# Kernel tuning notes

Measured on AMD Instinct MI355X. Metric: run time of the kernel, lower is better.

Reference implementation:

```python
import jax, jax.numpy as jnp
import numpy as np

B, HW, C, H = 4, 2048, 768, 8
HD = C // H  # 96


def _rotate_half_interleaved(t):
    # t: [..., HD]; pairs (t1, t2) at even/odd positions -> (-t2, t1) interleaved
    t1 = t[..., ::2]
    t2 = t[..., 1::2]
    return jnp.stack([-t2, t1], axis=-1).reshape(t.shape)


def setup_inputs() -> dict:
    key = jax.random.key(0)
    kx, kq, kp, kb = jax.random.split(key, 4)
    x = jax.random.normal(kx, (B, HW, C), dtype=jnp.float32)
    # standard interleaved RoPE tables: freq repeated pairwise along head_dim
    inv_freq = 1.0 / (10000.0 ** (np.arange(0, HD, 2, dtype=np.float32) / HD))  # [HD/2]
    angles = np.arange(HW, dtype=np.float32)[:, None] * inv_freq[None, :]        # [HW, HD/2]
    angles = np.repeat(angles, 2, axis=-1)                                        # [HW, HD]
    cos = jnp.asarray(np.cos(angles), dtype=jnp.float32)
    sin = jnp.asarray(np.sin(angles), dtype=jnp.float32)
    Wqkv = jax.random.normal(kq, (3 * C, C), dtype=jnp.float32) * (C ** -0.5)
    Wproj = jax.random.normal(kp, (C, C), dtype=jnp.float32) * (C ** -0.5)
    bproj = jnp.zeros((C,), dtype=jnp.float32)
    return {"x": x, "cos": cos, "sin": sin, "Wqkv": Wqkv, "Wproj": Wproj, "bproj": bproj}


def reference(x, cos, sin, Wqkv, Wproj, bproj):
    Bv, hw, Cv = x.shape
    scale = HD ** -0.5
    qkv = x @ Wqkv.T                                  # [B, hw, 3C]
    qkv = qkv.reshape(Bv, hw, 3, H, HD).transpose(2, 0, 3, 1, 4)  # [3, B, H, hw, HD]
    q, k, v = qkv[0], qkv[1], qkv[2]
    # RoPE: broadcast cos/sin [hw, HD] over [B, H, hw, HD]
    cosb = cos[None, None, :, :]
    sinb = sin[None, None, :, :]
    q = q * cosb + _rotate_half_interleaved(q) * sinb
    k = k * cosb + _rotate_half_interleaved(k) * sinb
    attn = jnp.einsum('bhqd,bhkd->bhqk', q, k) * scale
    attn = jax.nn.softmax(attn, axis=-1)
    out = jnp.einsum('bhqk,bhkd->bhqd', attn, v)      # [B, H, hw, HD]
    out = out.transpose(0, 2, 1, 3).reshape(Bv, hw, Cv)
    return out @ Wproj.T + bproj
```

## Files before the change

### kernel.cpp

```cpp
#include <hip/hip_runtime.h>
#include <hip/hip_bf16.h>
#include <math.h>

#define Bc  4
#define HWc 2048
#define Cc  768
#define Hc  8
#define HDc 96

typedef short bf16x8 __attribute__((ext_vector_type(8)));
typedef float f32x4  __attribute__((ext_vector_type(4)));

static __device__ __forceinline__ unsigned short f2bf(float x) {
    __hip_bfloat16 h = __float2bfloat16(x);
    return *reinterpret_cast<unsigned short*>(&h);
}

#define GLOBAL_AS(p) ((const __attribute__((address_space(1))) void*)(p))
#define LDS_AS(p)    ((__attribute__((address_space(3))) void*)(p))

__global__ __launch_bounds__(256) void cast_bf16(
    const float* __restrict__ src, unsigned short* __restrict__ dst, int n4)
{
    int i = blockIdx.x * 256 + threadIdx.x;
    if (i < n4) {
        float4 v = ((const float4*)src)[i];
        ushort4 p;
        p.x = f2bf(v.x); p.y = f2bf(v.y); p.z = f2bf(v.z); p.w = f2bf(v.w);
        ((ushort4*)dst)[i] = p;
    }
}

__global__ __launch_bounds__(256) void qkv_mfma_T(
    const unsigned short* __restrict__ Wb, const unsigned short* __restrict__ xb,
    const float* __restrict__ cs, const float* __restrict__ sn,
    unsigned short* __restrict__ qo, unsigned short* __restrict__ ko,
    unsigned short* __restrict__ vt)
{
    __shared__ unsigned short Al[128 * 32];
    __shared__ unsigned short Bl[128 * 32];
    const int tid  = threadIdx.x;
    const int lane = tid & 63;
    const int w    = tid >> 6;
    const int c    = lane & 15, qd = lane >> 4;
    const int wm   = w & 1, wn = w >> 1;
    const int m0   = blockIdx.y << 7;
    const int n0   = blockIdx.x << 7;

    const int srow = (w << 5) + (lane >> 2);
    const int sseg = (lane & 3) << 3;
    const unsigned short* Ag = Wb + (size_t)(m0 + srow) * Cc + sseg;
    const unsigned short* Bg = xb + (size_t)(n0 + srow) * Cc + sseg;
    unsigned short* Adst = &Al[(w << 5) * 32];
    unsigned short* Bdst = &Bl[(w << 5) * 32];

    f32x4 acc[4][4];
    #pragma unroll
    for (int i = 0; i < 4; i++)
        #pragma unroll
        for (int j = 0; j < 4; j++) acc[i][j] = (f32x4)0.f;

    for (int k0 = 0; k0 < Cc; k0 += 32) {
        __syncthreads();
        __builtin_amdgcn_global_load_lds(GLOBAL_AS(Ag + k0),            LDS_AS(Adst),            16, 0, 0);
        __builtin_amdgcn_global_load_lds(GLOBAL_AS(Ag + 16 * Cc + k0),  LDS_AS(Adst + 16 * 32),  16, 0, 0);
        __builtin_amdgcn_global_load_lds(GLOBAL_AS(Bg + k0),            LDS_AS(Bdst),            16, 0, 0);
        __builtin_amdgcn_global_load_lds(GLOBAL_AS(Bg + 16 * Cc + k0),  LDS_AS(Bdst + 16 * 32),  16, 0, 0);
        __syncthreads();

        bf16x8 af[4], bfr[4];
        #pragma unroll
        for (int mt = 0; mt < 4; mt++)
            af[mt] = *(const bf16x8*)&Al[((wm << 6) + mt * 16 + c) * 32 + qd * 8];
        #pragma unroll
        for (int nt = 0; nt < 4; nt++)
            bfr[nt] = *(const bf16x8*)&Bl[((wn << 6) + nt * 16 + c) * 32 + qd * 8];
        #pragma unroll
        for (int mt = 0; mt < 4; mt++)
            #pragma unroll
            for (int nt = 0; nt < 4; nt++)
                acc[mt][nt] = __builtin_amdgcn_mfma_f32_16x16x32_bf16(
                    af[mt], bfr[nt], acc[mt][nt], 0, 0, 0);
    }

    const int which = m0 / Cc;
    const int m0l = m0 - which * Cc;
    const float qs = 0.10206207261596577f;

    if (which == 2) {
        #pragma unroll
        for (int mt = 0; mt < 4; mt++) {
            const int c0 = m0l + (wm << 6) + mt * 16 + (qd << 2);
            const int h = c0 / HDc, d = c0 % HDc;
            #pragma unroll
            for (int nt = 0; nt < 4; nt++) {
                const int t = n0 + (wn << 6) + nt * 16 + c;
                const int b = t >> 11, tt = t & (HWc - 1);
                const size_t base = ((size_t)((b * Hc + h) * HDc + d)) * HWc + tt;
                #pragma unroll
                for (int r = 0; r < 4; r++)
                    vt[base + (size_t)r * HWc] = f2bf(acc[mt][nt][r]);
            }
        }
    } else {
        unsigned short* dst = which ? ko : qo;
        const float sc = which ? 1.0f : qs;
        #pragma unroll
        for (int mt = 0; mt < 4; mt++) {
            const int c0 = m0l + (wm << 6) + mt * 16 + (qd << 2);
            const int h = c0 / HDc, d = c0 % HDc;
            #pragma unroll
            for (int nt = 0; nt < 4; nt++) {
                const int t = n0 + (wn << 6) + nt * 16 + c;
                const int b = t >> 11, tt = t & (HWc - 1);
                const float4 c4 = *(const float4*)&cs[tt * HDc + d];
                const float4 s4 = *(const float4*)&sn[tt * HDc + d];
                float o0 = (acc[mt][nt][0] * c4.x - acc[mt][nt][1] * s4.x) * sc;
                float o1 = (acc[mt][nt][1] * c4.y + acc[mt][nt][0] * s4.y) * sc;
                float o2 = (acc[mt][nt][2] * c4.z - acc[mt][nt][3] * s4.z) * sc;
                float o3 = (acc[mt][nt][3] * c4.w + acc[mt][nt][2] * s4.w) * sc;
                ushort4 pk;
                pk.x = f2bf(o0); pk.y = f2bf(o1); pk.z = f2bf(o2); pk.w = f2bf(o3);
                *(ushort4*)&dst[((size_t)(b * Hc + h) * HWc + tt) * HDc + d] = pk;
            }
        }
    }
}

__global__ __launch_bounds__(256) void attn_flash(
    const unsigned short* __restrict__ qg, const unsigned short* __restrict__ kg,
    const unsigned short* __restrict__ vtg, unsigned short* __restrict__ ob)
{
    __shared__ unsigned short Ks[64][104];
    __shared__ unsigned short Vt[96][104];
    __shared__ unsigned short Pt[4][32][104];

    const int tid  = threadIdx.x;
    const int lane = tid & 63;
    const int w    = tid >> 6;
    const int c    = lane & 15;
    const int qd   = lane >> 4;
    const int bh   = blockIdx.x;
    const int b    = bh >> 3, h = bh & 7;
    const int q0   = blockIdx.y << 7;

    const unsigned short* kb  = kg  + (size_t)bh * HWc * HDc;
    const unsigned short* vtb = vtg + (size_t)bh * HDc * HWc;

    bf16x8 qt[2][3];
    #pragma unroll
    for (int nt = 0; nt < 2; nt++) {
        const unsigned short* qr =
            qg + ((size_t)bh * HWc + q0 + w * 32 + nt * 16 + c) * HDc + qd * 8;
        #pragma unroll
        for (int ks = 0; ks < 3; ks++)
            qt[nt][ks] = *(const bf16x8*)(qr + ks * 32);
    }

    f32x4 oacc[6][2];
    #pragma unroll
    for (int mt = 0; mt < 6; mt++)
        #pragma unroll
        for (int nt = 0; nt < 2; nt++) oacc[mt][nt] = (f32x4)0.f;
    float lsum[2] = {0.f, 0.f};

    const int krow0 = tid / 12,       kseg0 = tid - krow0 * 12;
    const int krow1 = (tid + 256) / 12, kseg1 = (tid + 256) - krow1 * 12;
    const int krow2 = (tid + 512) / 12, kseg2 = (tid + 512) - krow2 * 12;
    uint4 kreg[3], vreg[3];

    {
        const unsigned short* kc = kb;
        kreg[0] = *(const uint4*)(kc + krow0 * HDc + kseg0 * 8);
        kreg[1] = *(const uint4*)(kc + krow1 * HDc + kseg1 * 8);
        kreg[2] = *(const uint4*)(kc + krow2 * HDc + kseg2 * 8);
        const unsigned short* vc = vtb;
        #pragma unroll
        for (int it = 0; it < 3; it++) {
            int idx = tid + (it << 8);
            int row = idx >> 3, seg = idx & 7;
            vreg[it] = *(const uint4*)(vc + (size_t)row * HWc + seg * 8);
        }
    }

    for (int ck = 0; ck < 32; ck++) {
        __syncthreads();
        *(uint4*)&Ks[krow0][kseg0 * 8] = kreg[0];
        *(uint4*)&Ks[krow1][kseg1 * 8] = kreg[1];
        *(uint4*)&Ks[krow2][kseg2 * 8] = kreg[2];
        #pragma unroll
        for (int it = 0; it < 3; it++) {
            int idx = tid + (it << 8);
            int row = idx >> 3, seg = idx & 7;
            *(uint4*)&Vt[row][seg * 8] = vreg[it];
        }
        __syncthreads();

        if (ck + 1 < 32) {
            const unsigned short* kc = kb + (size_t)((ck + 1) << 6) * HDc;
            kreg[0] = *(const uint4*)(kc + krow0 * HDc + kseg0 * 8);
            kreg[1] = *(const uint4*)(kc + krow1 * HDc + kseg1 * 8);
            kreg[2] = *(const uint4*)(kc + krow2 * HDc + kseg2 * 8);
            const unsigned short* vc = vtb + ((ck + 1) << 6);
            #pragma unroll
            for (int it = 0; it < 3; it++) {
                int idx = tid + (it << 8);
                int row = idx >> 3, seg = idx & 7;
                vreg[it] = *(const uint4*)(vc + (size_t)row * HWc + seg * 8);
            }
        }

        f32x4 sacc[4][2];
        #pragma unroll
        for (int mt = 0; mt < 4; mt++)
            #pragma unroll
            for (int nt = 0; nt < 2; nt++) sacc[mt][nt] = (f32x4)0.f;
        #pragma unroll
        for (int mt = 0; mt < 4; mt++)
            #pragma unroll
            for (int ks = 0; ks < 3; ks++) {
                bf16x8 af = *(const bf16x8*)&Ks[mt * 16 + c][ks * 32 + qd * 8];
                sacc[mt][0] = __builtin_amdgcn_mfma_f32_16x16x32_bf16(
                    af, qt[0][ks], sacc[mt][0], 0, 0, 0);
                sacc[mt][1] = __builtin_amdgcn_mfma_f32_16x16x32_bf16(
                    af, qt[1][ks], sacc[mt][1], 0, 0, 0);
            }

        #pragma unroll
        for (int nt = 0; nt < 2; nt++) {
            float rs = 0.f;
            #pragma unroll
            for (int mt = 0; mt < 4; mt++)
                #pragma unroll
                for (int r = 0; r < 4; r++) {
                    float p = __expf(sacc[mt][nt][r]);
                    sacc[mt][nt][r] = p;
                    rs += p;
                }
            rs += __shfl_xor(rs, 16);
            rs += __shfl_xor(rs, 32);
            lsum[nt] += rs;
        }

        #pragma unroll
        for (int nt = 0; nt < 2; nt++)
            #pragma unroll
            for (int mt = 0; mt < 4; mt++) {
                __hip_bfloat162 p01 = __float22bfloat162_rn(
                    float2{sacc[mt][nt][0], sacc[mt][nt][1]});
                __hip_bfloat162 p23 = __float22bfloat162_rn(
                    float2{sacc[mt][nt][2], sacc[mt][nt][3]});
                uint2 pk;
                pk.x = *reinterpret_cast<unsigned int*>(&p01);
                pk.y = *reinterpret_cast<unsigned int*>(&p23);
                *(uint2*)&Pt[w][nt * 16 + c][mt * 16 + qd * 4] = pk;
            }
        bf16x8 pf[2][2];
        #pragma unroll
        for (int nt = 0; nt < 2; nt++)
            #pragma unroll
            for (int ks = 0; ks < 2; ks++)
                pf[nt][ks] = *(const bf16x8*)&Pt[w][nt * 16 + c][ks * 32 + qd * 8];

        #pragma unroll
        for (int mt = 0; mt < 6; mt++)
            #pragma unroll
            for (int ks = 0; ks < 2; ks++) {
                bf16x8 vf = *(const bf16x8*)&Vt[mt * 16 + c][ks * 32 + qd * 8];
                oacc[mt][0] = __builtin_amdgcn_mfma_f32_16x16x32_bf16(
                    vf, pf[0][ks], oacc[mt][0], 0, 0, 0);
                oacc[mt][1] = __builtin_amdgcn_mfma_f32_16x16x32_bf16(
                    vf, pf[1][ks], oacc[mt][1], 0, 0, 0);
            }
    }

    #pragma unroll
    for (int nt = 0; nt < 2; nt++) {
        const float linv = 1.0f / lsum[nt];
        unsigned short* orow =
            ob + ((size_t)(b * HWc + q0 + w * 32 + nt * 16 + c)) * Cc + h * HDc;
        #pragma unroll
        for (int mt = 0; mt < 6; mt++) {
            f32x4 val = oacc[mt][nt] * linv;
            ushort4 pk;
            pk.x = f2bf(val[0]); pk.y = f2bf(val[1]);
            pk.z = f2bf(val[2]); pk.w = f2bf(val[3]);
            *(ushort4*)&orow[mt * 16 + qd * 4] = pk;
        }
    }
}

__global__ __launch_bounds__(256) void proj_mfma_T(
    const unsigned short* __restrict__ Wb, const unsigned short* __restrict__ Ab,
    const float* __restrict__ bias, float* __restrict__ out)
{
    __shared__ unsigned short Al[128 * 32];
    __shared__ unsigned short Bl[128 * 32];
    const int tid  = threadIdx.x;
    const int lane = tid & 63;
    const int w    = tid >> 6;
    const int c    = lane & 15, qd = lane >> 4;
    const int wm   = w & 1, wn = w >> 1;
    const int m0   = blockIdx.y << 7;
    const int n0   = blockIdx.x << 7;

    const int srow = (w << 5) + (lane >> 2);
    const int sseg = (lane & 3) << 3;
    const unsigned short* Ag = Wb + (size_t)(m0 + srow) * Cc + sseg;
    const unsigned short* Bg = Ab + (size_t)(n0 + srow) * Cc + sseg;
    unsigned short* Adst = &Al[(w << 5) * 32];
    unsigned short* Bdst = &Bl[(w << 5) * 32];

    f32x4 acc[4][4];
    #pragma unroll
    for (int i = 0; i < 4; i++)
        #pragma unroll
        for (int j = 0; j < 4; j++) acc[i][j] = (f32x4)0.f;

    for (int k0 = 0; k0 < Cc; k0 += 32) {
        __syncthreads();
        __builtin_amdgcn_global_load_lds(GLOBAL_AS(Ag + k0),           LDS_AS(Adst),           16, 0, 0);
        __builtin_amdgcn_global_load_lds(GLOBAL_AS(Ag + 16 * Cc + k0), LDS_AS(Adst + 16 * 32), 16, 0, 0);
        __builtin_amdgcn_global_load_lds(GLOBAL_AS(Bg + k0),           LDS_AS(Bdst),           16, 0, 0);
        __builtin_amdgcn_global_load_lds(GLOBAL_AS(Bg + 16 * Cc + k0), LDS_AS(Bdst + 16 * 32), 16, 0, 0);
        __syncthreads();

        bf16x8 af[4], bfr[4];
        #pragma unroll
        for (int mt = 0; mt < 4; mt++)
            af[mt] = *(const bf16x8*)&Al[((wm << 6) + mt * 16 + c) * 32 + qd * 8];
        #pragma unroll
        for (int nt = 0; nt < 4; nt++)
            bfr[nt] = *(const bf16x8*)&Bl[((wn << 6) + nt * 16 + c) * 32 + qd * 8];
        #pragma unroll
        for (int mt = 0; mt < 4; mt++)
            #pragma unroll
            for (int nt = 0; nt < 4; nt++)
                acc[mt][nt] = __builtin_amdgcn_mfma_f32_16x16x32_bf16(
                    af[mt], bfr[nt], acc[mt][nt], 0, 0, 0);
    }

    #pragma unroll
    for (int mt = 0; mt < 4; mt++) {
        const int f = m0 + (wm << 6) + mt * 16 + (qd << 2);
        const float4 b4 = *(const float4*)&bias[f];
        #pragma unroll
        for (int nt = 0; nt < 4; nt++) {
            const int t = n0 + (wn << 6) + nt * 16 + c;
            float4 val;
            val.x = acc[mt][nt][0] + b4.x;
            val.y = acc[mt][nt][1] + b4.y;
            val.z = acc[mt][nt][2] + b4.z;
            val.w = acc[mt][nt][3] + b4.w;
            *(float4*)&out[(size_t)t * Cc + f] = val;
        }
    }
}

extern "C" void kernel_launch(void* const* d_in, const int* in_sizes, int n_in,
                              void* d_out, int out_size, void* d_ws, size_t ws_size,
                              hipStream_t stream) {
    const float* x     = (const float*)d_in[0];
    const float* cs    = (const float*)d_in[1];
    const float* sn    = (const float*)d_in[2];
    const float* Wqkv  = (const float*)d_in[3];
    const float* Wproj = (const float*)d_in[4];
    const float* bproj = (const float*)d_in[5];
    float* out = (float*)d_out;

    const size_t per = (size_t)Bc * Hc * HWc * HDc;
    const size_t nx  = per;
    const size_t nwq = (size_t)3 * Cc * Cc;
    const size_t nwp = (size_t)Cc * Cc;

    unsigned short* xb  = (unsigned short*)d_ws;
    unsigned short* Wqb = xb + nx;
    unsigned short* Wpb = Wqb + nwq;
    unsigned short* q   = Wpb + nwp;
    unsigned short* k   = q + per;
    unsigned short* vt  = k + per;
    unsigned short* ob  = vt + per;

    cast_bf16<<<dim3((int)(nx / 4 + 255) / 256), 256, 0, stream>>>(x, xb, (int)(nx / 4));
    cast_bf16<<<dim3((int)(nwq / 4 + 255) / 256), 256, 0, stream>>>(Wqkv, Wqb, (int)(nwq / 4));
    cast_bf16<<<dim3((int)(nwp / 4 + 255) / 256), 256, 0, stream>>>(Wproj, Wpb, (int)(nwp / 4));

    qkv_mfma_T<<<dim3(64, 18), 256, 0, stream>>>(Wqb, xb, cs, sn, q, k, vt);
    attn_flash<<<dim3(32, 16), 256, 0, stream>>>(q, k, vt, ob);
    proj_mfma_T<<<dim3(64, 6), 256, 0, stream>>>(Wpb, ob, bproj, out);
}
```

Before: 304.4 us.

## Shrink attention blocks to 128 threads and fuse the three cast kernels

The three fp32-to-bf16 cast launches are merged into one kernel that picks its source and destination by index range, removing two launches. The attention kernel is resized to 128 threads (2 waves) covering 64 queries per block, with the grid doubled to 32x32 and LDS padding shrunk to 72 columns, so each block uses less LDS and more blocks can be resident. Each thread now stages 6 K/V chunks instead of 3, which raises register pressure, and K/V tiles are loaded twice as often across the grid.

Measured after the change: 409.0 us. 34.4% more time.

```diff
diff --git a/kernel.cpp b/kernel.cpp
--- a/kernel.cpp
+++ b/kernel.cpp
@@ -19,16 +19,22 @@
 #define GLOBAL_AS(p) ((const __attribute__((address_space(1))) void*)(p))
 #define LDS_AS(p)    ((__attribute__((address_space(3))) void*)(p))
 
-__global__ __launch_bounds__(256) void cast_bf16(
-    const float* __restrict__ src, unsigned short* __restrict__ dst, int n4)
+__global__ __launch_bounds__(256) void cast_all(
+    const float* __restrict__ x, const float* __restrict__ Wq,
+    const float* __restrict__ Wp, unsigned short* __restrict__ xb,
+    unsigned short* __restrict__ Wqb, unsigned short* __restrict__ Wpb,
+    int nx4, int nwq4, int nwp4)
 {
     int i = blockIdx.x * 256 + threadIdx.x;
-    if (i < n4) {
-        float4 v = ((const float4*)src)[i];
-        ushort4 p;
-        p.x = f2bf(v.x); p.y = f2bf(v.y); p.z = f2bf(v.z); p.w = f2bf(v.w);
-        ((ushort4*)dst)[i] = p;
-    }
+    const float* src; unsigned short* dst; int j = i;
+    if (i < nx4) { src = x; dst = xb; }
+    else if ((j = i - nx4) < nwq4) { src = Wq; dst = Wqb; }
+    else if ((j = i - nx4 - nwq4) < nwp4) { src = Wp; dst = Wpb; }
+    else return;
+    float4 v = ((const float4*)src)[j];
+    ushort4 p;
+    p.x = f2bf(v.x); p.y = f2bf(v.y); p.z = f2bf(v.z); p.w = f2bf(v.w);
+    ((ushort4*)dst)[j] = p;
 }
 
 __global__ __launch_bounds__(256) void qkv_mfma_T(
@@ -127,13 +133,13 @@
     }
 }
 
-__global__ __launch_bounds__(256) void attn_flash(
+__global__ __launch_bounds__(128, 2) void attn_flash(
     const unsigned short* __restrict__ qg, const unsigned short* __restrict__ kg,
     const unsigned short* __restrict__ vtg, unsigned short* __restrict__ ob)
 {
     __shared__ unsigned short Ks[64][104];
-    __shared__ unsigned short Vt[96][104];
-    __shared__ unsigned short Pt[4][32][104];
+    __shared__ unsigned short Vt[96][72];
+    __shared__ unsigned short Pt[2][32][72];
 
     const int tid  = threadIdx.x;
     const int lane = tid & 63;
@@ -142,7 +148,7 @@
     const int qd   = lane >> 4;
     const int bh   = blockIdx.x;
     const int b    = bh >> 3, h = bh & 7;
-    const int q0   = blockIdx.y << 7;
+    const int q0   = blockIdx.y << 6;
 
     const unsigned short* kb  = kg  + (size_t)bh * HWc * HDc;
     const unsigned short* vtb = vtg + (size_t)bh * HDc * HWc;
@@ -164,33 +170,34 @@
         for (int nt = 0; nt < 2; nt++) oacc[mt][nt] = (f32x4)0.f;
     float lsum[2] = {0.f, 0.f};
 
-    const int krow0 = tid / 12,       kseg0 = tid - krow0 * 12;
-    const int krow1 = (tid + 256) / 12, kseg1 = (tid + 256) - krow1 * 12;
-    const int krow2 = (tid + 512) / 12, kseg2 = (tid + 512) - krow2 * 12;
-    uint4 kreg[3], vreg[3];
+    int krow[6], kseg[6];
+    #pragma unroll
+    for (int it = 0; it < 6; it++) {
+        int idx = tid + (it << 7);
+        krow[it] = idx / 12; kseg[it] = idx - krow[it] * 12;
+    }
+    uint4 kreg[6], vreg[6];
 
     {
-        const unsigned short* kc = kb;
-        kreg[0] = *(const uint4*)(kc + krow0 * HDc + kseg0 * 8);
-        kreg[1] = *(const uint4*)(kc + krow1 * HDc + kseg1 * 8);
-        kreg[2] = *(const uint4*)(kc + krow2 * HDc + kseg2 * 8);
-        const unsigned short* vc = vtb;
-        #pragma unroll
-        for (int it = 0; it < 3; it++) {
-            int idx = tid + (it << 8);
+        #pragma unroll
+        for (int it = 0; it < 6; it++)
+            kreg[it] = *(const uint4*)(kb + krow[it] * HDc + kseg[it] * 8);
+        #pragma unroll
+        for (int it = 0; it < 6; it++) {
+            int idx = tid + (it << 7);
             int row = idx >> 3, seg = idx & 7;
-            vreg[it] = *(const uint4*)(vc + (size_t)row * HWc + seg * 8);
+            vreg[it] = *(const uint4*)(vtb + (size_t)row * HWc + seg * 8);
         }
     }
 
     for (int ck = 0; ck < 32; ck++) {
         __syncthreads();
-        *(uint4*)&Ks[krow0][kseg0 * 8] = kreg[0];
-        *(uint4*)&Ks[krow1][kseg1 * 8] = kreg[1];
-        *(uint4*)&Ks[krow2][kseg2 * 8] = kreg[2];
-        #pragma unroll
-        for (int it = 0; it < 3; it++) {
-            int idx = tid + (it << 8);
+        #pragma unroll
+        for (int it = 0; it < 6; it++)
+            *(uint4*)&Ks[krow[it]][kseg[it] * 8] = kreg[it];
+        #pragma unroll
+        for (int it = 0; it < 6; it++) {
+            int idx = tid + (it << 7);
             int row = idx >> 3, seg = idx & 7;
             *(uint4*)&Vt[row][seg * 8] = vreg[it];
         }
@@ -198,13 +205,13 @@
 
         if (ck + 1 < 32) {
             const unsigned short* kc = kb + (size_t)((ck + 1) << 6) * HDc;
-            kreg[0] = *(const uint4*)(kc + krow0 * HDc + kseg0 * 8);
-            kreg[1] = *(const uint4*)(kc + krow1 * HDc + kseg1 * 8);
-            kreg[2] = *(const uint4*)(kc + krow2 * HDc + kseg2 * 8);
+            #pragma unroll
+            for (int it = 0; it < 6; it++)
+                kreg[it] = *(const uint4*)(kc + krow[it] * HDc + kseg[it] * 8);
             const unsigned short* vc = vtb + ((ck + 1) << 6);
             #pragma unroll
-            for (int it = 0; it < 3; it++) {
-                int idx = tid + (it << 8);
+            for (int it = 0; it < 6; it++) {
+                int idx = tid + (it << 7);
                 int row = idx >> 3, seg = idx & 7;
                 vreg[it] = *(const uint4*)(vc + (size_t)row * HWc + seg * 8);
             }
@@ -381,11 +388,12 @@
     unsigned short* vt  = k + per;
     unsigned short* ob  = vt + per;
 
-    cast_bf16<<<dim3((int)(nx / 4 + 255) / 256), 256, 0, stream>>>(x, xb, (int)(nx / 4));
-    cast_bf16<<<dim3((int)(nwq / 4 + 255) / 256), 256, 0, stream>>>(Wqkv, Wqb, (int)(nwq / 4));
-    cast_bf16<<<dim3((int)(nwp / 4 + 255) / 256), 256, 0, stream>>>(Wproj, Wpb, (int)(nwp / 4));
+    const int nx4 = (int)(nx / 4), nwq4 = (int)(nwq / 4), nwp4 = (int)(nwp / 4);
+    const int ntot = nx4 + nwq4 + nwp4;
+    cast_all<<<dim3((ntot + 255) / 256), 256, 0, stream>>>(
+        x, Wqkv, Wproj, xb, Wqb, Wpb, nx4, nwq4, nwp4);
 
     qkv_mfma_T<<<dim3(64, 18), 256, 0, stream>>>(Wqb, xb, cs, sn, q, k, vt);
-    attn_flash<<<dim3(32, 16), 256, 0, stream>>>(q, k, vt, ob);
+    attn_flash<<<dim3(32, 32), 128, 0, stream>>>(q, k, vt, ob);
     proj_mfma_T<<<dim3(64, 6), 256, 0, stream>>>(Wpb, ob, bproj, out);
 }
```
